# Kernel optimization log

Measured on AMD Instinct MI355X. Metric: run time of the kernel, lower is better.

## Reference

```python
import jax, jax.numpy as jnp
import numpy as np

B, S, N, M = 2, 4, 4096, 4096


def setup_inputs() -> dict:
    key = jax.random.key(0)
    k1, k2 = jax.random.split(key)
    output_points = jax.random.normal(k1, (B, S, N, 3), dtype=jnp.float32)
    target_points = jax.random.normal(k2, (B, S, M, 3), dtype=jnp.float32)
    return {"output_points": output_points, "target_points": target_points, "n_samples": N}


def _chamfer(x, y):
    # x: [B,S,N,3], y: [B,S,M,3]; squared-Euclidean bidirectional NN distances
    x2 = jnp.sum(x * x, axis=-1)                      # [B,S,N]
    y2 = jnp.sum(y * y, axis=-1)                      # [B,S,M]
    xy = jnp.einsum('bsnd,bsmd->bsnm', x, y)          # [B,S,N,M]
    d = x2[..., :, None] + y2[..., None, :] - 2.0 * xy
    dist1 = jnp.min(d, axis=-1)                       # [B,S,N] out->tgt NN
    dist2 = jnp.min(d, axis=-2)                       # [B,S,M] tgt->out NN
    return dist1, dist2


def reference(output_points, target_points, n_samples):
    # n_samples already applied (clouds are pre-sampled to fixed size)
    dist1, dist2 = _chamfer(output_points, target_points)
    # per-(b,s) combined distance: mean(dist1) + mean(dist2)
    combined = jnp.mean(dist1, axis=-1) + jnp.mean(dist2, axis=-1)  # [B,S]
    chamfer_distances_tensor = combined.T                            # [S,B]
    chamfer_distances = jnp.mean(chamfer_distances_tensor, axis=1)   # [S] (dict s -> mean over batch)
    return chamfer_distances, chamfer_distances_tensor
```

## Files before the change

### kernel.cpp

```cpp
#include <hip/hip_runtime.h>

constexpr int Sn = 4;
constexpr int Nn = 4096;
constexpr int Mn = 4096;
constexpr int NS2 = 16;
constexpr int CH  = 8;


template <int APT, int NBC>
__global__ __launch_bounds__(256) void chamfer_partial(
    const float* __restrict__ X,
    const float* __restrict__ Y,
    float* __restrict__ pmin)
{
    constexpr int BCHUNK = Mn / NBC;
    constexpr int ATILE  = APT * 256;

    __shared__ float4 ldsB[BCHUNK];

    const int at    = blockIdx.x;
    const int bc    = blockIdx.y;
    const int z     = blockIdx.z;
    const int slice = z & 7;
    const int dir   = z >> 3;
    const int tid   = threadIdx.x;

    const float* A  = (dir == 0 ? X : Y) + slice * (Nn * 3);
    const float* Bp = (dir == 0 ? Y : X) + slice * (Mn * 3) + bc * (BCHUNK * 3);

    float ax[APT], ay[APT], az[APT], a2[APT], acc[APT];
    #pragma unroll
    for (int j = 0; j < APT; ++j) {
        const int n = at * ATILE + j * 256 + tid;
        ax[j] = A[n * 3 + 0];
        ay[j] = A[n * 3 + 1];
        az[j] = A[n * 3 + 2];
        a2[j] = ax[j] * ax[j] + ay[j] * ay[j] + az[j] * az[j];
        acc[j] = 3.4e38f;
    }

    for (int p = tid; p < BCHUNK; p += 256) {
        float bx = Bp[p * 3 + 0], by = Bp[p * 3 + 1], bz = Bp[p * 3 + 2];
        ldsB[p] = make_float4(-2.0f * bx, -2.0f * by, -2.0f * bz,
                              bx * bx + by * by + bz * bz);
    }
    __syncthreads();

    #pragma unroll 4
    for (int m = 0; m < BCHUNK; m += 2) {
        float4 b0 = ldsB[m + 0];
        float4 b1 = ldsB[m + 1];
        #pragma unroll
        for (int j = 0; j < APT; ++j) {
            float d0 = fmaf(ax[j], b0.x, fmaf(ay[j], b0.y, fmaf(az[j], b0.z, b0.w)));
            float d1 = fmaf(ax[j], b1.x, fmaf(ay[j], b1.y, fmaf(az[j], b1.z, b1.w)));
            acc[j] = fminf(acc[j], fminf(d0, d1));
        }
    }

    float* dst = pmin + ((size_t)z * NBC + bc) * Nn + at * ATILE;
    #pragma unroll
    for (int j = 0; j < APT; ++j) dst[j * 256 + tid] = acc[j] + a2[j];
}

template <int NBC>
__global__ __launch_bounds__(256) void chamfer_combine(
    const float* __restrict__ pmin, float* __restrict__ sums2)
{
    const int z   = blockIdx.x;
    const int c   = blockIdx.y;
    const int tid = threadIdx.x;
    constexpr int SPAN = Nn / CH;

    const float* p = pmin + (size_t)z * NBC * Nn;

    float s = 0.0f;
    for (int i = c * SPAN + tid; i < (c + 1) * SPAN; i += 256) {
        float m = p[i];
        #pragma unroll
        for (int bc = 1; bc < NBC; ++bc) m = fminf(m, p[(size_t)bc * Nn + i]);
        s += m;
    }

    s += __shfl_down(s, 32);
    s += __shfl_down(s, 16);
    s += __shfl_down(s, 8);
    s += __shfl_down(s, 4);
    s += __shfl_down(s, 2);
    s += __shfl_down(s, 1);

    __shared__ float red[4];
    if ((tid & 63) == 0) red[tid >> 6] = s;
    __syncthreads();
    if (tid == 0) sums2[z * CH + c] = red[0] + red[1] + red[2] + red[3];
}

__global__ __launch_bounds__(64) void chamfer_finalize(
    const float* __restrict__ sums2, float* __restrict__ out)
{
    const int tid = threadIdx.x;
    __shared__ float tot[NS2];
    if (tid < NS2) {
        float t = 0.0f;
        #pragma unroll
        for (int c = 0; c < CH; ++c) t += sums2[tid * CH + c];
        tot[tid] = t;
    }
    __syncthreads();
    if (tid < 8) {
        const int s = tid >> 1, b = tid & 1;
        const int l = b * Sn + s;
        out[4 + s * 2 + b] = tot[l] * (1.0f / Nn) + tot[8 + l] * (1.0f / Mn);
    } else if (tid < 12) {
        const int s = tid - 8;
        float c0 = tot[0 * Sn + s] * (1.0f / Nn) + tot[8 + 0 * Sn + s] * (1.0f / Mn);
        float c1 = tot[1 * Sn + s] * (1.0f / Nn) + tot[8 + 1 * Sn + s] * (1.0f / Mn);
        out[s] = 0.5f * (c0 + c1);
    }
}

extern "C" void kernel_launch(void* const* d_in, const int* in_sizes, int n_in,
                              void* d_out, int out_size, void* d_ws, size_t ws_size,
                              hipStream_t stream) {
    const float* X = (const float*)d_in[0];
    const float* Y = (const float*)d_in[1];
    float* out  = (float*)d_out;
    float* pmin = (float*)d_ws;

    const size_t need_main = ((size_t)NS2 * 32 * Nn + 256) * sizeof(float);

    if (ws_size >= need_main) {
        constexpr int APT = 8, NBC = 32;
        float* sums2 = pmin + (size_t)NS2 * NBC * Nn;
        dim3 grid(Nn / (APT * 256), NBC, NS2);
        chamfer_partial<APT, NBC><<<grid, 256, 0, stream>>>(X, Y, pmin);
        chamfer_combine<NBC><<<dim3(NS2, CH), 256, 0, stream>>>(pmin, sums2);
        chamfer_finalize<<<1, 64, 0, stream>>>(sums2, out);
    } else {
        constexpr int APT = 4, NBC = 4;
        float* sums2 = pmin + (size_t)NS2 * NBC * Nn;
        dim3 grid(Nn / (APT * 256), NBC, NS2);
        chamfer_partial<APT, NBC><<<grid, 256, 0, stream>>>(X, Y, pmin);
        chamfer_combine<NBC><<<dim3(NS2, CH), 256, 0, stream>>>(pmin, sums2);
        chamfer_finalize<<<1, 64, 0, stream>>>(sums2, out);
    }
}
```

Measured before the change: 34.71 us.

## Increase points per thread, split B into more chunks, vectorize A loads and stores

Each thread now holds 16 query points instead of 8, and the reference cloud is split into 64 chunks instead of 32. Query points are loaded and partial minima stored as contiguous float4 per thread rather than strided scalars. The combine stage uses more chunks per slice, with a bounded unroll and a launch-bounds occupancy hint. The aim is to reuse each shared-memory B point across more FMAs and to cut global load instructions. In exchange the partial-minimum workspace doubles, register pressure rises, and the per-thread float4 accesses lose cross-lane coalescing.

```diff
diff --git a/kernel.cpp b/kernel.cpp
--- a/kernel.cpp
+++ b/kernel.cpp
@@ -4,17 +4,18 @@
 constexpr int Nn = 4096;
 constexpr int Mn = 4096;
 constexpr int NS2 = 16;
-constexpr int CH  = 8;
+constexpr int CH  = 16;
 
 
 template <int APT, int NBC>
-__global__ __launch_bounds__(256) void chamfer_partial(
+__global__ __launch_bounds__(256, 4) void chamfer_partial(
     const float* __restrict__ X,
     const float* __restrict__ Y,
     float* __restrict__ pmin)
 {
     constexpr int BCHUNK = Mn / NBC;
     constexpr int ATILE  = APT * 256;
+    static_assert(APT % 4 == 0, "APT multiple of 4 for float4 A-loads");
 
     __shared__ float4 ldsB[BCHUNK];
 
@@ -29,14 +30,23 @@
     const float* Bp = (dir == 0 ? Y : X) + slice * (Mn * 3) + bc * (BCHUNK * 3);
 
     float ax[APT], ay[APT], az[APT], a2[APT], acc[APT];
+    const float4* A4 = (const float4*)(A + (size_t)(at * ATILE + tid * APT) * 3);
     #pragma unroll
-    for (int j = 0; j < APT; ++j) {
-        const int n = at * ATILE + j * 256 + tid;
-        ax[j] = A[n * 3 + 0];
-        ay[j] = A[n * 3 + 1];
-        az[j] = A[n * 3 + 2];
-        a2[j] = ax[j] * ax[j] + ay[j] * ay[j] + az[j] * az[j];
-        acc[j] = 3.4e38f;
+    for (int g = 0; g < APT / 4; ++g) {
+        float4 q0 = A4[3 * g + 0];
+        float4 q1 = A4[3 * g + 1];
+        float4 q2 = A4[3 * g + 2];
+        float c[12] = {q0.x, q0.y, q0.z, q0.w, q1.x, q1.y, q1.z, q1.w,
+                       q2.x, q2.y, q2.z, q2.w};
+        #pragma unroll
+        for (int k = 0; k < 4; ++k) {
+            const int j = 4 * g + k;
+            ax[j] = c[3 * k + 0];
+            ay[j] = c[3 * k + 1];
+            az[j] = c[3 * k + 2];
+            a2[j] = ax[j] * ax[j] + ay[j] * ay[j] + az[j] * az[j];
+            acc[j] = 3.4e38f;
+        }
     }
 
     for (int p = tid; p < BCHUNK; p += 256) {
@@ -58,9 +68,15 @@
         }
     }
 
-    float* dst = pmin + ((size_t)z * NBC + bc) * Nn + at * ATILE;
+    float* dstf = pmin + ((size_t)z * NBC + bc) * Nn + at * ATILE + tid * APT;
+    float4* dst4 = (float4*)dstf;
     #pragma unroll
-    for (int j = 0; j < APT; ++j) dst[j * 256 + tid] = acc[j] + a2[j];
+    for (int g = 0; g < APT / 4; ++g) {
+        dst4[g] = make_float4(acc[4 * g + 0] + a2[4 * g + 0],
+                              acc[4 * g + 1] + a2[4 * g + 1],
+                              acc[4 * g + 2] + a2[4 * g + 2],
+                              acc[4 * g + 3] + a2[4 * g + 3]);
+    }
 }
 
 template <int NBC>
@@ -77,7 +93,7 @@
     float s = 0.0f;
     for (int i = c * SPAN + tid; i < (c + 1) * SPAN; i += 256) {
         float m = p[i];
-        #pragma unroll
+        #pragma unroll 8
         for (int bc = 1; bc < NBC; ++bc) m = fminf(m, p[(size_t)bc * Nn + i]);
         s += m;
     }
@@ -127,10 +143,10 @@
     float* out  = (float*)d_out;
     float* pmin = (float*)d_ws;
 
-    const size_t need_main = ((size_t)NS2 * 32 * Nn + 256) * sizeof(float);
+    const size_t need_main = ((size_t)NS2 * 64 * Nn + NS2 * CH + 64) * sizeof(float);
 
     if (ws_size >= need_main) {
-        constexpr int APT = 8, NBC = 32;
+        constexpr int APT = 16, NBC = 64;
         float* sums2 = pmin + (size_t)NS2 * NBC * Nn;
         dim3 grid(Nn / (APT * 256), NBC, NS2);
         chamfer_partial<APT, NBC><<<grid, 256, 0, stream>>>(X, Y, pmin);
```

Measured after the change: 50.42 us. +45.3%, slower.
